# Performance work log

Hardware: AMD Instinct MI355X
Metric: run time of the kernel (lower is better)

## Reference

```python
import jax, jax.numpy as jnp
import numpy as np

DIM = 512
B, H_GRID, W_GRID = 16, 64, 64
N_TOKENS = 1 + H_GRID * W_GRID


def setup_inputs() -> dict:
    key = jax.random.key(0)
    ks = jax.random.split(key, 7)
    x = jax.random.normal(ks[0], (B, N_TOKENS, DIM), dtype=jnp.float32)
    # depthwise conv weights, torch layout [C_out, C_in/groups=1, k, k]
    w7 = jax.random.normal(ks[1], (DIM, 1, 7, 7), dtype=jnp.float32) * 0.02
    b7 = jax.random.normal(ks[2], (DIM,), dtype=jnp.float32) * 0.02
    w5 = jax.random.normal(ks[3], (DIM, 1, 5, 5), dtype=jnp.float32) * 0.02
    b5 = jax.random.normal(ks[4], (DIM,), dtype=jnp.float32) * 0.02
    w3 = jax.random.normal(ks[5], (DIM, 1, 3, 3), dtype=jnp.float32) * 0.02
    b3 = jax.random.normal(ks[6], (DIM,), dtype=jnp.float32) * 0.02
    return {"x": x, "w7": w7, "b7": b7, "w5": w5, "b5": b5,
            "w3": w3, "b3": b3, "H": H_GRID, "W": W_GRID}


def _dwconv(v, w, b, k):
    # depthwise same-padding conv, NCHW / OIHW, feature_group_count = channels
    p = k // 2
    C = v.shape[1]
    y = jax.lax.conv_general_dilated(
        v, w, window_strides=(1, 1), padding=[(p, p), (p, p)],
        dimension_numbers=("NCHW", "OIHW", "NCHW"),
        feature_group_count=C)
    return y + b[None, :, None, None]


def reference(x, w7, b7, w5, b5, w3, b3, H, W):
    Bsz, N, C = x.shape
    cls_token = x[:, :1]                         # [B, 1, C]
    feat_tokens = x[:, 1:]                       # [B, H*W, C]
    cnn_feat = feat_tokens.transpose(0, 2, 1).reshape(Bsz, C, H, W)
    x_conv = (_dwconv(cnn_feat, w7, b7, 7)
              + _dwconv(cnn_feat, w5, b5, 5)
              + _dwconv(cnn_feat, w3, b3, 3)
              + cnn_feat)
    feats = x_conv.reshape(Bsz, C, H * W).transpose(0, 2, 1)  # [B, H*W, C]
    return jnp.concatenate((cls_token, feats), axis=1)
```

## Files before the change

### kernel.cpp

```cpp
#include <hip/hip_runtime.h>

#define DIMC 512
#define NTOK 4097
#define GH 64
#define GW 64
#define TH 16

__global__ __launch_bounds__(256) void prep_kernel(
    const float* __restrict__ w7, const float* __restrict__ b7,
    const float* __restrict__ w5, const float* __restrict__ b5,
    const float* __restrict__ w3, const float* __restrict__ b3,
    float* __restrict__ wc, float* __restrict__ bc)
{
    int idx = blockIdx.x * 256 + threadIdx.x;
    if (idx < DIMC * 49) {
        int c = idx & (DIMC - 1);
        int t = idx >> 9;
        int dy = t / 7, dx = t - dy * 7;
        float v = w7[c * 49 + t];
        if (dy >= 1 && dy <= 5 && dx >= 1 && dx <= 5)
            v += w5[c * 25 + (dy - 1) * 5 + (dx - 1)];
        if (dy >= 2 && dy <= 4 && dx >= 2 && dx <= 4)
            v += w3[c * 9 + (dy - 2) * 3 + (dx - 2)];
        if (dy == 3 && dx == 3) v += 1.0f;
        wc[t * DIMC + c] = v;
    }
    if (idx < DIMC) bc[idx] = b7[idx] + b5[idx] + b3[idx];
}

__global__ __launch_bounds__(256) void cls_kernel(
    const float* __restrict__ x, float* __restrict__ out)
{
    int i = blockIdx.x * 256 + threadIdx.x;
    int b = i >> 9, c = i & 511;
    size_t off = (size_t)b * NTOK * DIMC + c;
    out[off] = x[off];
}

__global__ __launch_bounds__(256) void dwconv_kernel(
    const float* __restrict__ x, const float* __restrict__ wc,
    const float* __restrict__ bc, float* __restrict__ out)
{
    const int c_in_chunk = threadIdx.x;
    const int wlane = threadIdx.y;
    const int wseg = blockIdx.x;
    const int yid  = blockIdx.y;
    const int b    = blockIdx.z;
    const int cc = (yid >> 2) * 64 + c_in_chunk;
    const int h0 = (yid & 3) * TH;
    const int w  = wseg * 4 + wlane;

    float wgt[49];
#pragma unroll
    for (int t = 0; t < 49; ++t) wgt[t] = wc[t * DIMC + cc];
    const float bias = bc[cc];

    const float* __restrict__ xin = x   + ((size_t)b * NTOK + 1) * DIMC + cc;
    float* __restrict__ op        = out + ((size_t)b * NTOK + 1) * DIMC + cc;

    float win[7][7];

    auto load_row = [&](int r, float* row) {
        if (r < 0 || r >= GH) {
#pragma unroll
            for (int dx = 0; dx < 7; ++dx) row[dx] = 0.0f;
        } else {
            const float* rp = xin + (size_t)r * GW * DIMC;
#pragma unroll
            for (int dx = 0; dx < 7; ++dx) {
                int col = w - 3 + dx;
                row[dx] = (col >= 0 && col < GW) ? rp[(size_t)col * DIMC] : 0.0f;
            }
        }
    };

#pragma unroll
    for (int p = 0; p < 6; ++p) load_row(h0 - 3 + p, win[p]);

#pragma unroll
    for (int o = 0; o < TH; ++o) {
        load_row(h0 + o + 3, win[(o + 6) % 7]);
        float acc = bias;
#pragma unroll
        for (int dy = 0; dy < 7; ++dy) {
            const float* row = win[(o + dy) % 7];
#pragma unroll
            for (int dx = 0; dx < 7; ++dx)
                acc += wgt[dy * 7 + dx] * row[dx];
        }
        op[((size_t)(h0 + o) * GW + w) * DIMC] = acc;
    }
}

extern "C" void kernel_launch(void* const* d_in, const int* in_sizes, int n_in,
                              void* d_out, int out_size, void* d_ws, size_t ws_size,
                              hipStream_t stream)
{
    const float* x  = (const float*)d_in[0];
    const float* w7 = (const float*)d_in[1];
    const float* b7 = (const float*)d_in[2];
    const float* w5 = (const float*)d_in[3];
    const float* b5 = (const float*)d_in[4];
    const float* w3 = (const float*)d_in[5];
    const float* b3 = (const float*)d_in[6];
    float* out = (float*)d_out;
    float* wcomb = (float*)d_ws;
    float* bcomb = wcomb + 49 * DIMC;

    prep_kernel<<<98, 256, 0, stream>>>(w7, b7, w5, b5, w3, b3, wcomb, bcomb);
    cls_kernel<<<32, 256, 0, stream>>>(x, out);

    dim3 grid(16, 32, 16);
    dim3 block(64, 4, 1);
    dwconv_kernel<<<grid, block, 0, stream>>>(x, wcomb, bcomb, out);
}
```

Before: 346.9 us.

## Compute four output columns per thread with row-streaming accumulators

Each thread now produces a 4-wide by 16-tall output tile instead of one column. It streams one 10-wide input row at a time into a double buffer and scatters the row into up to 7 rolling accumulator rows. This cuts redundant global loads of overlapping input columns and rows, and the grid shrinks by a factor of four to match. The cost is higher register pressure from 28 accumulators plus 49 weights plus buffers, which may lower occupancy or cause spills.

```diff
diff --git a/kernel.cpp b/kernel.cpp
--- a/kernel.cpp
+++ b/kernel.cpp
@@ -41,14 +41,14 @@
     const float* __restrict__ x, const float* __restrict__ wc,
     const float* __restrict__ bc, float* __restrict__ out)
 {
-    const int c_in_chunk = threadIdx.x;
-    const int wlane = threadIdx.y;
+    const int lane = threadIdx.x;
+    const int wv   = threadIdx.y;
     const int wseg = blockIdx.x;
     const int yid  = blockIdx.y;
     const int b    = blockIdx.z;
-    const int cc = (yid >> 2) * 64 + c_in_chunk;
+    const int cc = (yid >> 2) * 64 + lane;
     const int h0 = (yid & 3) * TH;
-    const int w  = wseg * 4 + wlane;
+    const int w0 = (wseg * 4 + wv) * 4;
 
     float wgt[49];
 #pragma unroll
@@ -58,37 +58,55 @@
     const float* __restrict__ xin = x   + ((size_t)b * NTOK + 1) * DIMC + cc;
     float* __restrict__ op        = out + ((size_t)b * NTOK + 1) * DIMC + cc;
 
-    float win[7][7];
+    float acc[7][4];
+    float buf[2][10];
 
-    auto load_row = [&](int r, float* row) {
+    auto load_row = [&](int r, float (&row)[10]) {
         if (r < 0 || r >= GH) {
 #pragma unroll
-            for (int dx = 0; dx < 7; ++dx) row[dx] = 0.0f;
+            for (int i = 0; i < 10; ++i) row[i] = 0.0f;
         } else {
             const float* rp = xin + (size_t)r * GW * DIMC;
 #pragma unroll
-            for (int dx = 0; dx < 7; ++dx) {
-                int col = w - 3 + dx;
-                row[dx] = (col >= 0 && col < GW) ? rp[(size_t)col * DIMC] : 0.0f;
+            for (int i = 0; i < 10; ++i) {
+                int ci = w0 - 3 + i;
+                row[i] = (ci >= 0 && ci < GW) ? rp[(size_t)ci * DIMC] : 0.0f;
             }
         }
     };
 
-#pragma unroll
-    for (int p = 0; p < 6; ++p) load_row(h0 - 3 + p, win[p]);
+    load_row(h0 - 3, buf[0]);
 
 #pragma unroll
-    for (int o = 0; o < TH; ++o) {
-        load_row(h0 + o + 3, win[(o + 6) % 7]);
-        float acc = bias;
+    for (int k = 0; k < TH + 6; ++k) {
+        float (&cur)[10] = buf[k & 1];
+        if (k + 1 < TH + 6) load_row(h0 - 3 + (k + 1), buf[(k + 1) & 1]);
+
+        if (k <= TH - 1) {
 #pragma unroll
-        for (int dy = 0; dy < 7; ++dy) {
-            const float* row = win[(o + dy) % 7];
+            for (int c = 0; c < 4; ++c) acc[k % 7][c] = bias;
+        }
+
 #pragma unroll
-            for (int dx = 0; dx < 7; ++dx)
-                acc += wgt[dy * 7 + dx] * row[dx];
+        for (int j = 0; j < TH; ++j) {
+            if (j >= ((k - 6 < 0) ? 0 : k - 6) && j <= ((k < TH - 1) ? k : TH - 1)) {
+                const int dy = k - j;
+#pragma unroll
+                for (int c = 0; c < 4; ++c) {
+#pragma unroll
+                    for (int dx = 0; dx < 7; ++dx)
+                        acc[j % 7][c] += wgt[dy * 7 + dx] * cur[c + dx];
+                }
+            }
         }
-        op[((size_t)(h0 + o) * GW + w) * DIMC] = acc;
+
+        if (k >= 6) {
+            const int j = k - 6;
+            const int o = h0 + j;
+#pragma unroll
+            for (int c = 0; c < 4; ++c)
+                op[((size_t)o * GW + (w0 + c)) * DIMC] = acc[j % 7][c];
+        }
     }
 }
 
@@ -110,7 +128,7 @@
     prep_kernel<<<98, 256, 0, stream>>>(w7, b7, w5, b5, w3, b3, wcomb, bcomb);
     cls_kernel<<<32, 256, 0, stream>>>(x, out);
 
-    dim3 grid(16, 32, 16);
+    dim3 grid(4, 32, 16);
     dim3 block(64, 4, 1);
     dwconv_kernel<<<grid, block, 0, stream>>>(x, wcomb, bcomb, out);
 }
```

After: 402.0 us. 1.16x slower.
